# Performance work log

Hardware: AMD Instinct MI355X
Metric: run time of the kernel (lower is better)

The kernel has to match this reference:

```python
import jax, jax.numpy as jnp
import numpy as np

N_NODES = 50000
N_EDGES = 800000
D_IN, D_HID, D_OUT = 128, 128, 256
EPS = 1e-12  # F.normalize eps


def _mean_aggr(h, src, dst, n):
    # scatter-mean of source features onto destination nodes
    msg_sum = jax.ops.segment_sum(h[src], dst, num_segments=n)
    deg = jax.ops.segment_sum(jnp.ones((src.shape[0],), h.dtype), dst, num_segments=n)
    return msg_sum / jnp.maximum(deg, 1.0)[:, None]


def _l2_normalize(h):
    # F.normalize(p=2, dim=1): divide by clamped L2 norm
    nrm = jnp.sqrt(jnp.sum(h * h, axis=1, keepdims=True))
    return h / jnp.maximum(nrm, EPS)


def setup_inputs() -> dict:
    key = jax.random.key(0)
    ks = jax.random.split(key, 8)
    x = jax.random.normal(ks[0], (N_NODES, D_IN), dtype=jnp.float32)
    edge_index = jax.random.randint(ks[1], (2, N_EDGES), 0, N_NODES, dtype=jnp.int64 if jax.config.read('jax_enable_x64') else jnp.int32)
    s = 1.0 / np.sqrt(D_IN)
    W1_l = jax.random.uniform(ks[2], (D_IN, D_HID), jnp.float32, -s, s)
    W1_r = jax.random.uniform(ks[3], (D_IN, D_HID), jnp.float32, -s, s)
    b1 = jnp.zeros((D_HID,), jnp.float32)
    s2 = 1.0 / np.sqrt(D_HID)
    W2_l = jax.random.uniform(ks[4], (D_HID, D_OUT), jnp.float32, -s2, s2)
    W2_r = jax.random.uniform(ks[5], (D_HID, D_OUT), jnp.float32, -s2, s2)
    b2 = jnp.zeros((D_OUT,), jnp.float32)
    return {"x": x, "edge_index": edge_index, "W1_l": W1_l, "W1_r": W1_r,
            "b1": b1, "W2_l": W2_l, "W2_r": W2_r, "b2": b2}


def reference(x, edge_index, W1_l, W1_r, b1, W2_l, W2_r, b2):
    src, dst = edge_index[0], edge_index[1]
    n = x.shape[0]
    # SAGEConv 1: lin_l(mean_aggr(x)) + lin_r(x) + bias
    h = _mean_aggr(x, src, dst, n) @ W1_l + x @ W1_r + b1
    # dropout is identity in eval mode
    h = _l2_normalize(jax.nn.sigmoid(h))
    # SAGEConv 2
    h = _mean_aggr(h, src, dst, n) @ W2_l + h @ W2_r + b2
    h = _l2_normalize(jax.nn.sigmoid(h))
    return jax.nn.log_softmax(h, axis=-1)
```

## Files before the change

kernel.cpp:

```cpp
#include <hip/hip_runtime.h>

#define NN 50000
#define NE 800000
#define NB 782
#define CAP 1536


__device__ __forceinline__ unsigned short f2bf(float f) {
    union { float f; unsigned u; } v; v.f = f;
    unsigned u = v.u;
    return (unsigned short)((u + 0x7fffu + ((u >> 16) & 1u)) >> 16);
}
__device__ __forceinline__ float bfu_lo(unsigned p) {
    union { unsigned u; float f; } v; v.u = p << 16; return v.f;
}
__device__ __forceinline__ float bfu_hi(unsigned p) {
    union { unsigned u; float f; } v; v.u = p & 0xffff0000u; return v.f;
}

typedef __bf16 bf16x8 __attribute__((ext_vector_type(8)));
typedef float f32x4 __attribute__((ext_vector_type(4)));
union U16 { uint4 u; bf16x8 v; };


__global__ __launch_bounds__(512) void binscatter_kernel(const int* __restrict__ src,
                                                         const int* __restrict__ dst,
                                                         int* __restrict__ bcnt,
                                                         unsigned* __restrict__ ebuf) {
    __shared__ int hist[NB];
    __shared__ int base[NB];
    const int BE = 8192;
    int tid = threadIdx.x;
    int e0 = blockIdx.x * BE;
    for (int i = tid; i < NB; i += 512) hist[i] = 0;
    __syncthreads();
    for (int i = tid; i < BE; i += 512) {
        int e = e0 + i;
        if (e < NE) atomicAdd(&hist[dst[e] >> 6], 1);
    }
    __syncthreads();
    for (int i = tid; i < NB; i += 512) {
        int c = hist[i];
        base[i] = c ? atomicAdd(&bcnt[i], c) : 0;
        hist[i] = 0;
    }
    __syncthreads();
    for (int i = tid; i < BE; i += 512) {
        int e = e0 + i;
        if (e < NE) {
            int d = dst[e], b = d >> 6;
            int slot = base[b] + atomicAdd(&hist[b], 1);
            if (slot < CAP)
                ebuf[(size_t)b * CAP + slot] = (unsigned)src[e] | ((unsigned)(d & 63) << 16);
        }
    }
}

__global__ __launch_bounds__(256) void csr_kernel(const int* __restrict__ bcnt,
                                                  const unsigned* __restrict__ ebuf,
                                                  int* __restrict__ rowptr,
                                                  int* __restrict__ col) {
    __shared__ int red[256];
    __shared__ int deg[64];
    __shared__ int cur[64];
    __shared__ int cbase_s;
    int b = blockIdx.x, tid = threadIdx.x;
    int s = 0;
    for (int i = tid; i < b; i += 256) s += bcnt[i];
    red[tid] = s;
    if (tid < 64) deg[tid] = 0;
    __syncthreads();
    for (int off = 128; off; off >>= 1) {
        if (tid < off) red[tid] += red[tid + off];
        __syncthreads();
    }
    if (tid == 0) cbase_s = red[0];
    __syncthreads();
    int cnt = bcnt[b], cbase = cbase_s;
    if (cnt > CAP) cnt = CAP;
    const unsigned* eb = ebuf + (size_t)b * CAP;
    for (int i = tid; i < cnt; i += 256) atomicAdd(&deg[(eb[i] >> 16) & 63], 1);
    __syncthreads();
    if (tid == 0) {
        int run = 0;
        for (int j = 0; j < 64; j++) { cur[j] = run; run += deg[j]; }
    }
    __syncthreads();
    int node = b * 64 + tid;
    if (tid < 64 && node < NN) rowptr[node] = cbase + cur[tid];
    if (b == NB - 1 && tid == 0) rowptr[NN] = NE;
    __syncthreads();
    for (int i = tid; i < cnt; i += 256) {
        unsigned e = eb[i];
        int pos = atomicAdd(&cur[(e >> 16) & 63], 1);
        col[cbase + pos] = (int)(e & 0xffffu);
    }
}


template <int N>
__device__ __forceinline__ void pack_one(const float* __restrict__ Wl,
                                         const float* __restrict__ Wr,
                                         unsigned short* __restrict__ Wp, int t) {
    int lane = t & 63, c = t >> 6;
    int ks = c & 7, nt = c >> 3;
    int n = nt * 16 + (lane & 15);
    int kq = ks * 32 + (lane >> 4) * 8;
    unsigned short tmp[8];
#pragma unroll
    for (int j = 0; j < 8; j++) {
        int k = kq + j;
        float w = (k < 128) ? Wl[(size_t)k * N + n] : Wr[(size_t)(k - 128) * N + n];
        tmp[j] = f2bf(w);
    }
    ((ushort4*)Wp)[(size_t)c * 128 + lane * 2 + 0] = make_ushort4(tmp[0], tmp[1], tmp[2], tmp[3]);
    ((ushort4*)Wp)[(size_t)c * 128 + lane * 2 + 1] = make_ushort4(tmp[4], tmp[5], tmp[6], tmp[7]);
}

#define CAST_BLK (NN * 128 / 4 / 256)

__global__ void castpack_kernel(const float* __restrict__ in, unsigned short* __restrict__ outp,
                                const float* __restrict__ W1l, const float* __restrict__ W1r,
                                unsigned short* __restrict__ W1p,
                                const float* __restrict__ W2l, const float* __restrict__ W2r,
                                unsigned short* __restrict__ W2p) {
    if (blockIdx.x < CAST_BLK) {
        int i = blockIdx.x * 256 + threadIdx.x;
        float4 f = ((const float4*)in)[i];
        ushort4 o;
        o.x = f2bf(f.x); o.y = f2bf(f.y); o.z = f2bf(f.z); o.w = f2bf(f.w);
        ((ushort4*)outp)[i] = o;
    } else {
        int t = (blockIdx.x - CAST_BLK) * 256 + threadIdx.x;
        if (t < 8 * 8 * 64) pack_one<128>(W1l, W1r, W1p, t);
        else if (t < 8 * 8 * 64 + 16 * 8 * 64) pack_one<256>(W2l, W2r, W2p, t - 8 * 8 * 64);
    }
}


__global__ void aggregate_bf_kernel(const int* __restrict__ rowptr, const int* __restrict__ col,
                                    const uint4* __restrict__ feat4,
                                    uint4* __restrict__ out4) {
    int wid = (blockIdx.x * blockDim.x + threadIdx.x) >> 6;
    int lane = threadIdx.x & 63;
    if (wid >= NN) return;
    int beg = rowptr[wid], end = rowptr[wid + 1];
    int deg = end - beg;
    int g = lane >> 4, c16 = lane & 15;
    int nmain = deg < 64 ? deg : 64;
    int cidx = (lane < nmain) ? col[beg + lane] : 0;
    float acc[8];
#pragma unroll
    for (int j = 0; j < 8; j++) acc[j] = 0.f;
    for (int i = 0; i < nmain; i += 8) {
        int e0 = i + g, e1 = i + 4 + g;
        int s0 = __shfl(cidx, e0);
        int s1 = __shfl(cidx, e1);
        uint4 v0 = make_uint4(0u, 0u, 0u, 0u);
        uint4 v1 = make_uint4(0u, 0u, 0u, 0u);
        if (e0 < nmain) v0 = feat4[(size_t)s0 * 16 + c16];
        if (e1 < nmain) v1 = feat4[(size_t)s1 * 16 + c16];
        acc[0] += bfu_lo(v0.x); acc[1] += bfu_hi(v0.x);
        acc[2] += bfu_lo(v0.y); acc[3] += bfu_hi(v0.y);
        acc[4] += bfu_lo(v0.z); acc[5] += bfu_hi(v0.z);
        acc[6] += bfu_lo(v0.w); acc[7] += bfu_hi(v0.w);
        acc[0] += bfu_lo(v1.x); acc[1] += bfu_hi(v1.x);
        acc[2] += bfu_lo(v1.y); acc[3] += bfu_hi(v1.y);
        acc[4] += bfu_lo(v1.z); acc[5] += bfu_hi(v1.z);
        acc[6] += bfu_lo(v1.w); acc[7] += bfu_hi(v1.w);
    }
    for (int i = 64; i < deg; i += 4) {
        int idx = beg + i + g;
        if (idx < end) {
            int s = col[idx];
            uint4 v = feat4[(size_t)s * 16 + c16];
            acc[0] += bfu_lo(v.x); acc[1] += bfu_hi(v.x);
            acc[2] += bfu_lo(v.y); acc[3] += bfu_hi(v.y);
            acc[4] += bfu_lo(v.z); acc[5] += bfu_hi(v.z);
            acc[6] += bfu_lo(v.w); acc[7] += bfu_hi(v.w);
        }
    }
#pragma unroll
    for (int j = 0; j < 8; j++) {
        acc[j] += __shfl_xor(acc[j], 16);
        acc[j] += __shfl_xor(acc[j], 32);
    }
    if (g == 0) {
        float inv = (deg > 0) ? 1.0f / (float)deg : 0.0f;
        uint4 o;
        o.x = (unsigned)f2bf(acc[0] * inv) | ((unsigned)f2bf(acc[1] * inv) << 16);
        o.y = (unsigned)f2bf(acc[2] * inv) | ((unsigned)f2bf(acc[3] * inv) << 16);
        o.z = (unsigned)f2bf(acc[4] * inv) | ((unsigned)f2bf(acc[5] * inv) << 16);
        o.w = (unsigned)f2bf(acc[6] * inv) | ((unsigned)f2bf(acc[7] * inv) << 16);
        out4[(size_t)wid * 16 + c16] = o;
    }
}


template <int N, bool FINAL>
__global__ __launch_bounds__(256) void gemm_mfma_kernel(
    const unsigned short* __restrict__ A0, const unsigned short* __restrict__ A1,
    const unsigned short* __restrict__ Wp, const float* __restrict__ bias,
    void* __restrict__ outp, int M) {
    const int NT = N / 16;
    int tid = threadIdx.x, wave = tid >> 6, lane = tid & 63;
    int quad = lane >> 4, col = lane & 15;
    int m_base = blockIdx.x * 64 + wave * 16;
    int row = m_base + col;
    int row_ld = row < M ? row : M - 1;

    bf16x8 a[8];
    const uint4* a0p = (const uint4*)(A0 + (size_t)row_ld * 128 + quad * 8);
    const uint4* a1p = (const uint4*)(A1 + (size_t)row_ld * 128 + quad * 8);
#pragma unroll
    for (int ks = 0; ks < 4; ks++) { U16 u; u.u = a0p[ks * 4]; a[ks] = u.v; }
#pragma unroll
    for (int ks = 0; ks < 4; ks++) { U16 u; u.u = a1p[ks * 4]; a[4 + ks] = u.v; }

    f32x4 acc[NT];
#pragma unroll
    for (int nt = 0; nt < NT; nt++) acc[nt] = (f32x4){0.f, 0.f, 0.f, 0.f};

    const uint4* wp = (const uint4*)Wp;
#pragma unroll
    for (int nt = 0; nt < NT; nt++) {
#pragma unroll
        for (int ks = 0; ks < 8; ks++) {
            U16 u; u.u = wp[(size_t)(nt * 8 + ks) * 64 + lane];
            acc[nt] = __builtin_amdgcn_mfma_f32_16x16x32_bf16(a[ks], u.v, acc[nt], 0, 0, 0);
        }
    }

    float ssq[4] = {0.f, 0.f, 0.f, 0.f};
#pragma unroll
    for (int nt = 0; nt < NT; nt++) {
        float bv = bias[nt * 16 + col];
#pragma unroll
        for (int r = 0; r < 4; r++) {
            float z = acc[nt][r] + bv;
            float s = 1.0f / (1.0f + __expf(-z));
            acc[nt][r] = s;
            ssq[r] += s * s;
        }
    }
#pragma unroll
    for (int r = 0; r < 4; r++) {
#pragma unroll
        for (int off = 1; off < 16; off <<= 1) ssq[r] += __shfl_xor(ssq[r], off, 16);
        float sc = 1.0f / fmaxf(sqrtf(ssq[r]), 1e-12f);
#pragma unroll
        for (int nt = 0; nt < NT; nt++) acc[nt][r] *= sc;
    }

    if (FINAL) {
#pragma unroll
        for (int r = 0; r < 4; r++) {
            float mx = -1e30f;
#pragma unroll
            for (int nt = 0; nt < NT; nt++) mx = fmaxf(mx, acc[nt][r]);
#pragma unroll
            for (int off = 1; off < 16; off <<= 1) mx = fmaxf(mx, __shfl_xor(mx, off, 16));
            float se = 0.f;
#pragma unroll
            for (int nt = 0; nt < NT; nt++) se += __expf(acc[nt][r] - mx);
#pragma unroll
            for (int off = 1; off < 16; off <<= 1) se += __shfl_xor(se, off, 16);
            float lse = mx + __logf(se);
#pragma unroll
            for (int nt = 0; nt < NT; nt++) acc[nt][r] -= lse;
        }
        float* op = (float*)outp;
#pragma unroll
        for (int r = 0; r < 4; r++) {
            int m = m_base + quad * 4 + r;
            if (m < M) {
#pragma unroll
                for (int nt = 0; nt < NT; nt++) op[(size_t)m * N + nt * 16 + col] = acc[nt][r];
            }
        }
    } else {
        unsigned short* op = (unsigned short*)outp;
#pragma unroll
        for (int r = 0; r < 4; r++) {
            int m = m_base + quad * 4 + r;
            if (m < M) {
#pragma unroll
                for (int nt = 0; nt < NT; nt++)
                    op[(size_t)m * N + nt * 16 + col] = f2bf(acc[nt][r]);
            }
        }
    }
}


extern "C" void kernel_launch(void* const* d_in, const int* in_sizes, int n_in,
                              void* d_out, int out_size, void* d_ws, size_t ws_size,
                              hipStream_t stream) {
    const float* x   = (const float*)d_in[0];
    const int*   ei  = (const int*)d_in[1];
    const float* W1l = (const float*)d_in[2];
    const float* W1r = (const float*)d_in[3];
    const float* b1  = (const float*)d_in[4];
    const float* W2l = (const float*)d_in[5];
    const float* W2r = (const float*)d_in[6];
    const float* b2  = (const float*)d_in[7];
    float* out = (float*)d_out;

    const int* src = ei;
    const int* dst = ei + NE;

    char* ws = (char*)d_ws;
    size_t off = 0;
    auto alloc = [&](size_t bytes) -> void* {
        void* p = ws + off;
        off += (bytes + 255) / 256 * 256;
        return p;
    };
    int* rowptr     = (int*)alloc((size_t)(NN + 1) * 4);
    int* col        = (int*)alloc((size_t)NE * 4);
    int* bcnt       = (int*)alloc((size_t)NB * 4);
    unsigned* ebuf  = (unsigned*)alloc((size_t)NB * CAP * 4);
    unsigned short* x_bf   = (unsigned short*)alloc((size_t)NN * 128 * 2);
    unsigned short* agg_bf = (unsigned short*)alloc((size_t)NN * 128 * 2);
    unsigned short* h1_bf  = (unsigned short*)alloc((size_t)NN * 128 * 2);
    unsigned short* W1p    = (unsigned short*)alloc((size_t)8 * 8 * 64 * 8 * 2);
    unsigned short* W2p    = (unsigned short*)alloc((size_t)16 * 8 * 64 * 8 * 2);

    hipMemsetAsync(bcnt, 0, (size_t)NB * 4, stream);
    binscatter_kernel<<<(NE + 8191) / 8192, 512, 0, stream>>>(src, dst, bcnt, ebuf);
    csr_kernel<<<NB, 256, 0, stream>>>(bcnt, ebuf, rowptr, col);

    castpack_kernel<<<CAST_BLK + 48, 256, 0, stream>>>(x, x_bf, W1l, W1r, W1p, W2l, W2r, W2p);

    aggregate_bf_kernel<<<(NN + 3) / 4, 256, 0, stream>>>(rowptr, col, (const uint4*)x_bf,
                                                          (uint4*)agg_bf);
    gemm_mfma_kernel<128, false><<<(NN + 63) / 64, 256, 0, stream>>>(agg_bf, x_bf, W1p, b1,
                                                                     h1_bf, NN);
    aggregate_bf_kernel<<<(NN + 3) / 4, 256, 0, stream>>>(rowptr, col, (const uint4*)h1_bf,
                                                          (uint4*)agg_bf);
    gemm_mfma_kernel<256, true><<<(NN + 63) / 64, 256, 0, stream>>>(agg_bf, h1_bf, W2p, b2,
                                                                    out, NN);
}
```

Measured before the change: 235.5 us.

## Split GEMM output columns across two waves with shared-memory row reductions

Each 16-row tile is now computed by two waves, each owning half of the output columns, so blocks grow to 512 threads and every wave holds half as many accumulators. Row-wise L2-norm and log-softmax statistics are combined across the two halves through shared memory with block barriers. The aim is lower register pressure, higher occupancy and more parallelism in the GEMM+epilogue kernels. The cost is that A rows are loaded twice (once per wave) and extra __syncthreads calls are added.

Result: no change. 239.8 us (+1.8%).

```diff
diff --git a/kernel.cpp b/kernel.cpp
--- a/kernel.cpp
+++ b/kernel.cpp
@@ -198,14 +198,19 @@
 
 
 template <int N, bool FINAL>
-__global__ __launch_bounds__(256) void gemm_mfma_kernel(
+__global__ __launch_bounds__(512) void gemm_mfma_kernel(
     const unsigned short* __restrict__ A0, const unsigned short* __restrict__ A1,
     const unsigned short* __restrict__ Wp, const float* __restrict__ bias,
     void* __restrict__ outp, int M) {
-    const int NT = N / 16;
+    const int NT = N / 32;
+    __shared__ float redS[2][64];
+    __shared__ float redM[2][64];
+    __shared__ float redE[2][64];
     int tid = threadIdx.x, wave = tid >> 6, lane = tid & 63;
+    int half = wave & 1;
+    int rg = wave >> 1;
     int quad = lane >> 4, col = lane & 15;
-    int m_base = blockIdx.x * 64 + wave * 16;
+    int m_base = blockIdx.x * 64 + rg * 16;
     int row = m_base + col;
     int row_ld = row < M ? row : M - 1;
 
@@ -226,15 +231,17 @@
     for (int nt = 0; nt < NT; nt++) {
 #pragma unroll
         for (int ks = 0; ks < 8; ks++) {
-            U16 u; u.u = wp[(size_t)(nt * 8 + ks) * 64 + lane];
+            U16 u; u.u = wp[(size_t)((half * NT + nt) * 8 + ks) * 64 + lane];
             acc[nt] = __builtin_amdgcn_mfma_f32_16x16x32_bf16(a[ks], u.v, acc[nt], 0, 0, 0);
         }
     }
 
+    int rbase = rg * 16 + quad * 4;
+
     float ssq[4] = {0.f, 0.f, 0.f, 0.f};
 #pragma unroll
     for (int nt = 0; nt < NT; nt++) {
-        float bv = bias[nt * 16 + col];
+        float bv = bias[half * (NT * 16) + nt * 16 + col];
 #pragma unroll
         for (int r = 0; r < 4; r++) {
             float z = acc[nt][r] + bv;
@@ -247,35 +254,58 @@
     for (int r = 0; r < 4; r++) {
 #pragma unroll
         for (int off = 1; off < 16; off <<= 1) ssq[r] += __shfl_xor(ssq[r], off, 16);
-        float sc = 1.0f / fmaxf(sqrtf(ssq[r]), 1e-12f);
+    }
+    if (col == 0) {
+#pragma unroll
+        for (int r = 0; r < 4; r++) redS[half][rbase + r] = ssq[r];
+    }
+    __syncthreads();
+#pragma unroll
+    for (int r = 0; r < 4; r++) {
+        float tot = redS[0][rbase + r] + redS[1][rbase + r];
+        float sc = 1.0f / fmaxf(sqrtf(tot), 1e-12f);
 #pragma unroll
         for (int nt = 0; nt < NT; nt++) acc[nt][r] *= sc;
     }
 
     if (FINAL) {
-#pragma unroll
-        for (int r = 0; r < 4; r++) {
-            float mx = -1e30f;
-#pragma unroll
-            for (int nt = 0; nt < NT; nt++) mx = fmaxf(mx, acc[nt][r]);
-#pragma unroll
-            for (int off = 1; off < 16; off <<= 1) mx = fmaxf(mx, __shfl_xor(mx, off, 16));
-            float se = 0.f;
-#pragma unroll
-            for (int nt = 0; nt < NT; nt++) se += __expf(acc[nt][r] - mx);
-#pragma unroll
-            for (int off = 1; off < 16; off <<= 1) se += __shfl_xor(se, off, 16);
-            float lse = mx + __logf(se);
-#pragma unroll
-            for (int nt = 0; nt < NT; nt++) acc[nt][r] -= lse;
-        }
+        float mx[4], se[4];
+#pragma unroll
+        for (int r = 0; r < 4; r++) {
+            mx[r] = -1e30f;
+#pragma unroll
+            for (int nt = 0; nt < NT; nt++) mx[r] = fmaxf(mx[r], acc[nt][r]);
+#pragma unroll
+            for (int off = 1; off < 16; off <<= 1) mx[r] = fmaxf(mx[r], __shfl_xor(mx[r], off, 16));
+        }
+        if (col == 0) {
+#pragma unroll
+            for (int r = 0; r < 4; r++) redM[half][rbase + r] = mx[r];
+        }
+        __syncthreads();
+#pragma unroll
+        for (int r = 0; r < 4; r++) {
+            mx[r] = fmaxf(redM[0][rbase + r], redM[1][rbase + r]);
+            se[r] = 0.f;
+#pragma unroll
+            for (int nt = 0; nt < NT; nt++) se[r] += __expf(acc[nt][r] - mx[r]);
+#pragma unroll
+            for (int off = 1; off < 16; off <<= 1) se[r] += __shfl_xor(se[r], off, 16);
+        }
+        if (col == 0) {
+#pragma unroll
+            for (int r = 0; r < 4; r++) redE[half][rbase + r] = se[r];
+        }
+        __syncthreads();
         float* op = (float*)outp;
 #pragma unroll
         for (int r = 0; r < 4; r++) {
+            float lse = mx[r] + __logf(redE[0][rbase + r] + redE[1][rbase + r]);
             int m = m_base + quad * 4 + r;
             if (m < M) {
 #pragma unroll
-                for (int nt = 0; nt < NT; nt++) op[(size_t)m * N + nt * 16 + col] = acc[nt][r];
+                for (int nt = 0; nt < NT; nt++)
+                    op[(size_t)m * N + half * (NT * 16) + nt * 16 + col] = acc[nt][r] - lse;
             }
         }
     } else {
@@ -286,7 +316,7 @@
             if (m < M) {
 #pragma unroll
                 for (int nt = 0; nt < NT; nt++)
-                    op[(size_t)m * N + nt * 16 + col] = f2bf(acc[nt][r]);
+                    op[(size_t)m * N + half * (NT * 16) + nt * 16 + col] = f2bf(acc[nt][r]);
             }
         }
     }
@@ -334,10 +364,10 @@
 
     aggregate_bf_kernel<<<(NN + 3) / 4, 256, 0, stream>>>(rowptr, col, (const uint4*)x_bf,
                                                           (uint4*)agg_bf);
-    gemm_mfma_kernel<128, false><<<(NN + 63) / 64, 256, 0, stream>>>(agg_bf, x_bf, W1p, b1,
+    gemm_mfma_kernel<128, false><<<(NN + 63) / 64, 512, 0, stream>>>(agg_bf, x_bf, W1p, b1,
                                                                      h1_bf, NN);
     aggregate_bf_kernel<<<(NN + 3) / 4, 256, 0, stream>>>(rowptr, col, (const uint4*)h1_bf,
                                                           (uint4*)agg_bf);
-    gemm_mfma_kernel<256, true><<<(NN + 63) / 64, 256, 0, stream>>>(agg_bf, h1_bf, W2p, b2,
+    gemm_mfma_kernel<256, true><<<(NN + 63) / 64, 512, 0, stream>>>(agg_bf, h1_bf, W2p, b2,
                                                                     out, NN);
 }
```

## Stage packed weights in LDS and compute two row tiles per wave in GEMM

Applied to the files above, without the earlier changes.

The GEMM kernel now copies the packed weight matrix into 64KB of shared memory with async global-to-LDS loads, in phases for the 256-wide layer. Each wave handles 32 rows instead of 16, so every weight fragment read from LDS feeds two MFMAs. The block now covers 128 rows, halving the grid. This is meant to cut repeated global/L2 weight fetches per row tile. The cost is higher register and LDS use, which lowers occupancy. The log-softmax also drops the max subtraction, relying on the inputs being L2-normalized sigmoid outputs in [0,1].

Measured after the change: 337.7 us. 43.4% more time.

```diff
diff --git a/kernel.cpp b/kernel.cpp
--- a/kernel.cpp
+++ b/kernel.cpp
@@ -21,6 +21,12 @@
 typedef __bf16 bf16x8 __attribute__((ext_vector_type(8)));
 typedef float f32x4 __attribute__((ext_vector_type(4)));
 union U16 { uint4 u; bf16x8 v; };
+
+typedef unsigned int u32_as1 __attribute__((address_space(1)));
+typedef unsigned int u32_as3 __attribute__((address_space(3)));
+__device__ __forceinline__ void gload_lds16(const void* g, void* l) {
+    __builtin_amdgcn_global_load_lds((const u32_as1*)g, (u32_as3*)l, 16, 0, 0);
+}
 
 
 __global__ __launch_bounds__(512) void binscatter_kernel(const int* __restrict__ src,
@@ -203,90 +209,122 @@
     const unsigned short* __restrict__ Wp, const float* __restrict__ bias,
     void* __restrict__ outp, int M) {
     const int NT = N / 16;
+    const int NPH = NT / 8;
+    __shared__ unsigned char sW[65536];
     int tid = threadIdx.x, wave = tid >> 6, lane = tid & 63;
     int quad = lane >> 4, col = lane & 15;
-    int m_base = blockIdx.x * 64 + wave * 16;
-    int row = m_base + col;
-    int row_ld = row < M ? row : M - 1;
-
-    bf16x8 a[8];
-    const uint4* a0p = (const uint4*)(A0 + (size_t)row_ld * 128 + quad * 8);
-    const uint4* a1p = (const uint4*)(A1 + (size_t)row_ld * 128 + quad * 8);
-#pragma unroll
-    for (int ks = 0; ks < 4; ks++) { U16 u; u.u = a0p[ks * 4]; a[ks] = u.v; }
-#pragma unroll
-    for (int ks = 0; ks < 4; ks++) { U16 u; u.u = a1p[ks * 4]; a[4 + ks] = u.v; }
-
-    f32x4 acc[NT];
-#pragma unroll
-    for (int nt = 0; nt < NT; nt++) acc[nt] = (f32x4){0.f, 0.f, 0.f, 0.f};
-
-    const uint4* wp = (const uint4*)Wp;
-#pragma unroll
-    for (int nt = 0; nt < NT; nt++) {
+    int m_base = blockIdx.x * 128 + wave * 32;
+
+    {
+        const char* gs = (const char*)Wp + wave * 16384;
+        char* ld = (char*)sW + wave * 16384;
+#pragma unroll
+        for (int j = 0; j < 16; j++) gload_lds16(gs + j * 1024 + lane * 16, ld + j * 1024);
+    }
+
+    bf16x8 a0[8], a1[8];
+    {
+        int r0 = m_base + col;      int r0c = r0 < M ? r0 : M - 1;
+        int r1 = m_base + 16 + col; int r1c = r1 < M ? r1 : M - 1;
+        const uint4* p00 = (const uint4*)(A0 + (size_t)r0c * 128 + quad * 8);
+        const uint4* p01 = (const uint4*)(A1 + (size_t)r0c * 128 + quad * 8);
+        const uint4* p10 = (const uint4*)(A0 + (size_t)r1c * 128 + quad * 8);
+        const uint4* p11 = (const uint4*)(A1 + (size_t)r1c * 128 + quad * 8);
+#pragma unroll
+        for (int ks = 0; ks < 4; ks++) { U16 u; u.u = p00[ks * 4]; a0[ks] = u.v; }
+#pragma unroll
+        for (int ks = 0; ks < 4; ks++) { U16 u; u.u = p01[ks * 4]; a0[4 + ks] = u.v; }
+#pragma unroll
+        for (int ks = 0; ks < 4; ks++) { U16 u; u.u = p10[ks * 4]; a1[ks] = u.v; }
+#pragma unroll
+        for (int ks = 0; ks < 4; ks++) { U16 u; u.u = p11[ks * 4]; a1[4 + ks] = u.v; }
+    }
+
+    f32x4 acc[2][NT];
+#pragma unroll
+    for (int t = 0; t < 2; t++)
+#pragma unroll
+        for (int nt = 0; nt < NT; nt++) acc[t][nt] = (f32x4){0.f, 0.f, 0.f, 0.f};
+
+#pragma unroll
+    for (int p = 0; p < NPH; p++) {
+        __syncthreads();
 #pragma unroll
         for (int ks = 0; ks < 8; ks++) {
-            U16 u; u.u = wp[(size_t)(nt * 8 + ks) * 64 + lane];
-            acc[nt] = __builtin_amdgcn_mfma_f32_16x16x32_bf16(a[ks], u.v, acc[nt], 0, 0, 0);
-        }
-    }
-
-    float ssq[4] = {0.f, 0.f, 0.f, 0.f};
-#pragma unroll
-    for (int nt = 0; nt < NT; nt++) {
-        float bv = bias[nt * 16 + col];
+#pragma unroll
+            for (int nt = 0; nt < 8; nt++) {
+                U16 u;
+                u.u = *(const uint4*)(sW + (nt * 8 + ks) * 1024 + lane * 16);
+                acc[0][p * 8 + nt] = __builtin_amdgcn_mfma_f32_16x16x32_bf16(
+                    a0[ks], u.v, acc[0][p * 8 + nt], 0, 0, 0);
+                acc[1][p * 8 + nt] = __builtin_amdgcn_mfma_f32_16x16x32_bf16(
+                    a1[ks], u.v, acc[1][p * 8 + nt], 0, 0, 0);
+            }
+        }
+        if (p + 1 < NPH) {
+            __syncthreads();
+            const char* gs = (const char*)Wp + (p + 1) * 65536 + wave * 16384;
+            char* ld = (char*)sW + wave * 16384;
+#pragma unroll
+            for (int j = 0; j < 16; j++) gload_lds16(gs + j * 1024 + lane * 16, ld + j * 1024);
+        }
+    }
+
+#pragma unroll
+    for (int t = 0; t < 2; t++) {
+        float ssq[4] = {0.f, 0.f, 0.f, 0.f};
+#pragma unroll
+        for (int nt = 0; nt < NT; nt++) {
+            float bv = bias[nt * 16 + col];
+#pragma unroll
+            for (int r = 0; r < 4; r++) {
+                float z = acc[t][nt][r] + bv;
+                float s = 1.0f / (1.0f + __expf(-z));
+                acc[t][nt][r] = s;
+                ssq[r] += s * s;
+            }
+        }
 #pragma unroll
         for (int r = 0; r < 4; r++) {
-            float z = acc[nt][r] + bv;
-            float s = 1.0f / (1.0f + __expf(-z));
-            acc[nt][r] = s;
-            ssq[r] += s * s;
-        }
-    }
-#pragma unroll
-    for (int r = 0; r < 4; r++) {
-#pragma unroll
-        for (int off = 1; off < 16; off <<= 1) ssq[r] += __shfl_xor(ssq[r], off, 16);
-        float sc = 1.0f / fmaxf(sqrtf(ssq[r]), 1e-12f);
-#pragma unroll
-        for (int nt = 0; nt < NT; nt++) acc[nt][r] *= sc;
-    }
-
-    if (FINAL) {
-#pragma unroll
-        for (int r = 0; r < 4; r++) {
-            float mx = -1e30f;
-#pragma unroll
-            for (int nt = 0; nt < NT; nt++) mx = fmaxf(mx, acc[nt][r]);
-#pragma unroll
-            for (int off = 1; off < 16; off <<= 1) mx = fmaxf(mx, __shfl_xor(mx, off, 16));
-            float se = 0.f;
-#pragma unroll
-            for (int nt = 0; nt < NT; nt++) se += __expf(acc[nt][r] - mx);
-#pragma unroll
-            for (int off = 1; off < 16; off <<= 1) se += __shfl_xor(se, off, 16);
-            float lse = mx + __logf(se);
-#pragma unroll
-            for (int nt = 0; nt < NT; nt++) acc[nt][r] -= lse;
-        }
-        float* op = (float*)outp;
-#pragma unroll
-        for (int r = 0; r < 4; r++) {
-            int m = m_base + quad * 4 + r;
-            if (m < M) {
-#pragma unroll
-                for (int nt = 0; nt < NT; nt++) op[(size_t)m * N + nt * 16 + col] = acc[nt][r];
-            }
-        }
-    } else {
-        unsigned short* op = (unsigned short*)outp;
-#pragma unroll
-        for (int r = 0; r < 4; r++) {
-            int m = m_base + quad * 4 + r;
-            if (m < M) {
-#pragma unroll
-                for (int nt = 0; nt < NT; nt++)
-                    op[(size_t)m * N + nt * 16 + col] = f2bf(acc[nt][r]);
+#pragma unroll
+            for (int off = 1; off < 16; off <<= 1) ssq[r] += __shfl_xor(ssq[r], off, 16);
+            float sc = 1.0f / fmaxf(sqrtf(ssq[r]), 1e-12f);
+#pragma unroll
+            for (int nt = 0; nt < NT; nt++) acc[t][nt][r] *= sc;
+        }
+
+        if (FINAL) {
+#pragma unroll
+            for (int r = 0; r < 4; r++) {
+                float se = 0.f;
+#pragma unroll
+                for (int nt = 0; nt < NT; nt++) se += __expf(acc[t][nt][r]);
+#pragma unroll
+                for (int off = 1; off < 16; off <<= 1) se += __shfl_xor(se, off, 16);
+                float lse = __logf(se);
+#pragma unroll
+                for (int nt = 0; nt < NT; nt++) acc[t][nt][r] -= lse;
+            }
+            float* op = (float*)outp;
+#pragma unroll
+            for (int r = 0; r < 4; r++) {
+                int m = m_base + t * 16 + quad * 4 + r;
+                if (m < M) {
+#pragma unroll
+                    for (int nt = 0; nt < NT; nt++)
+                        op[(size_t)m * N + nt * 16 + col] = acc[t][nt][r];
+                }
+            }
+        } else {
+            unsigned short* op = (unsigned short*)outp;
+#pragma unroll
+            for (int r = 0; r < 4; r++) {
+                int m = m_base + t * 16 + quad * 4 + r;
+                if (m < M) {
+#pragma unroll
+                    for (int nt = 0; nt < NT; nt++)
+                        op[(size_t)m * N + nt * 16 + col] = f2bf(acc[t][nt][r]);
+                }
             }
         }
     }
@@ -334,10 +372,10 @@
 
     aggregate_bf_kernel<<<(NN + 3) / 4, 256, 0, stream>>>(rowptr, col, (const uint4*)x_bf,
                                                           (uint4*)agg_bf);
-    gemm_mfma_kernel<128, false><<<(NN + 63) / 64, 256, 0, stream>>>(agg_bf, x_bf, W1p, b1,
-                                                                     h1_bf, NN);
+    gemm_mfma_kernel<128, false><<<(NN + 127) / 128, 256, 0, stream>>>(agg_bf, x_bf, W1p, b1,
+                                                                       h1_bf, NN);
     aggregate_bf_kernel<<<(NN + 3) / 4, 256, 0, stream>>>(rowptr, col, (const uint4*)h1_bf,
                                                           (uint4*)agg_bf);
-    gemm_mfma_kernel<256, true><<<(NN + 63) / 64, 256, 0, stream>>>(agg_bf, h1_bf, W2p, b2,
-                                                                    out, NN);
-}
+    gemm_mfma_kernel<256, true><<<(NN + 127) / 128, 256, 0, stream>>>(agg_bf, h1_bf, W2p, b2,
+                                                                      out, NN);
+}
```

## Stage packed weights in LDS via global_load_lds and drop softmax max pass

Applied to the files above, without the earlier changes.

Each GEMM block now copies the packed bf16 weight matrix into a 64KB LDS buffer with direct global-to-LDS loads. For N=256 this happens in two phases with barriers between them, and the MFMAs then read their weights from LDS instead of global memory. Launch bounds now request two blocks per CU. The final log-softmax also drops the max-subtraction pass, which relies on inputs already being L2-normalized into [0,1], so exp cannot overflow. The cost is extra barriers and heavy LDS use that limits occupancy.

Measured after the change: 222.5 us. 5.5% less time.

```diff
diff --git a/kernel.cpp b/kernel.cpp
--- a/kernel.cpp
+++ b/kernel.cpp
@@ -21,6 +21,12 @@
 typedef __bf16 bf16x8 __attribute__((ext_vector_type(8)));
 typedef float f32x4 __attribute__((ext_vector_type(4)));
 union U16 { uint4 u; bf16x8 v; };
+
+typedef unsigned int u32_as1 __attribute__((address_space(1)));
+typedef unsigned int u32_as3 __attribute__((address_space(3)));
+__device__ __forceinline__ void gload_lds16(const void* g, void* l) {
+    __builtin_amdgcn_global_load_lds((const u32_as1*)g, (u32_as3*)l, 16, 0, 0);
+}
 
 
 __global__ __launch_bounds__(512) void binscatter_kernel(const int* __restrict__ src,
@@ -198,17 +204,26 @@
 
 
 template <int N, bool FINAL>
-__global__ __launch_bounds__(256) void gemm_mfma_kernel(
+__global__ __launch_bounds__(256, 2) void gemm_mfma_kernel(
     const unsigned short* __restrict__ A0, const unsigned short* __restrict__ A1,
     const unsigned short* __restrict__ Wp, const float* __restrict__ bias,
     void* __restrict__ outp, int M) {
     const int NT = N / 16;
+    const int NPH = NT / 8;
+    __shared__ unsigned char sW[65536];
     int tid = threadIdx.x, wave = tid >> 6, lane = tid & 63;
     int quad = lane >> 4, col = lane & 15;
     int m_base = blockIdx.x * 64 + wave * 16;
     int row = m_base + col;
     int row_ld = row < M ? row : M - 1;
 
+    {
+        const char* gs = (const char*)Wp + wave * 16384;
+        char* ld = (char*)sW + wave * 16384;
+#pragma unroll
+        for (int j = 0; j < 16; j++) gload_lds16(gs + j * 1024 + lane * 16, ld + j * 1024);
+    }
+
     bf16x8 a[8];
     const uint4* a0p = (const uint4*)(A0 + (size_t)row_ld * 128 + quad * 8);
     const uint4* a1p = (const uint4*)(A1 + (size_t)row_ld * 128 + quad * 8);
@@ -221,13 +236,32 @@
 #pragma unroll
     for (int nt = 0; nt < NT; nt++) acc[nt] = (f32x4){0.f, 0.f, 0.f, 0.f};
 
-    const uint4* wp = (const uint4*)Wp;
-#pragma unroll
-    for (int nt = 0; nt < NT; nt++) {
+    __syncthreads();
+#pragma unroll
+    for (int ks = 0; ks < 8; ks++) {
+#pragma unroll
+        for (int nt = 0; nt < 8; nt++) {
+            U16 u; u.u = *(const uint4*)(sW + (nt * 8 + ks) * 1024 + lane * 16);
+            acc[nt] = __builtin_amdgcn_mfma_f32_16x16x32_bf16(a[ks], u.v, acc[nt], 0, 0, 0);
+        }
+    }
+
+    if constexpr (NPH == 2) {
+        __syncthreads();
+        {
+            const char* gs = (const char*)Wp + 65536 + wave * 16384;
+            char* ld = (char*)sW + wave * 16384;
+#pragma unroll
+            for (int j = 0; j < 16; j++) gload_lds16(gs + j * 1024 + lane * 16, ld + j * 1024);
+        }
+        __syncthreads();
 #pragma unroll
         for (int ks = 0; ks < 8; ks++) {
-            U16 u; u.u = wp[(size_t)(nt * 8 + ks) * 64 + lane];
-            acc[nt] = __builtin_amdgcn_mfma_f32_16x16x32_bf16(a[ks], u.v, acc[nt], 0, 0, 0);
+#pragma unroll
+            for (int nt = 0; nt < 8; nt++) {
+                U16 u; u.u = *(const uint4*)(sW + (nt * 8 + ks) * 1024 + lane * 16);
+                acc[8 + nt] = __builtin_amdgcn_mfma_f32_16x16x32_bf16(a[ks], u.v, acc[8 + nt], 0, 0, 0);
+            }
         }
     }
 
@@ -255,17 +289,12 @@
     if (FINAL) {
 #pragma unroll
         for (int r = 0; r < 4; r++) {
-            float mx = -1e30f;
-#pragma unroll
-            for (int nt = 0; nt < NT; nt++) mx = fmaxf(mx, acc[nt][r]);
-#pragma unroll
-            for (int off = 1; off < 16; off <<= 1) mx = fmaxf(mx, __shfl_xor(mx, off, 16));
             float se = 0.f;
 #pragma unroll
-            for (int nt = 0; nt < NT; nt++) se += __expf(acc[nt][r] - mx);
+            for (int nt = 0; nt < NT; nt++) se += __expf(acc[nt][r]);
 #pragma unroll
             for (int off = 1; off < 16; off <<= 1) se += __shfl_xor(se, off, 16);
-            float lse = mx + __logf(se);
+            float lse = __logf(se);
 #pragma unroll
             for (int nt = 0; nt < NT; nt++) acc[nt][r] -= lse;
         }
```
